# Kernel tuning notes

Measured on AMD Instinct MI355X. Metric: run time of the kernel, lower is better.

Reference implementation:

```python
import jax, jax.numpy as jnp
import numpy as np

N_NODES = 100_000
N_EDGES = 1_600_000
D_IN = 128
D_HID = 128
LN_EPS = 1e-5


def setup_inputs() -> dict:
    key = jax.random.key(0)
    k1, k2, k3 = jax.random.split(key, 3)
    x = jax.random.normal(k1, (N_NODES, D_IN), dtype=jnp.float32)
    edge_index = jax.random.randint(k2, (2, N_EDGES), 0, N_NODES, dtype=jnp.int32)
    # GCNConv linear weight (glorot-ish) and bias
    W = jax.random.normal(k3, (D_IN, D_HID), dtype=jnp.float32) * (1.0 / np.sqrt(D_IN))
    b = jnp.zeros((D_HID,), dtype=jnp.float32)
    # LayerNorm params
    gamma = jnp.ones((D_HID,), dtype=jnp.float32)
    beta = jnp.zeros((D_HID,), dtype=jnp.float32)
    return {"x": x, "edge_index": edge_index, "W": W, "b": b, "gamma": gamma, "beta": beta}


def reference(x, edge_index, W, b, gamma, beta):
    n = x.shape[0]
    # --- GCNConv: add self-loops, symmetric normalization ---
    loop = jnp.arange(n, dtype=edge_index.dtype)
    row = jnp.concatenate([edge_index[0], loop])  # source j
    col = jnp.concatenate([edge_index[1], loop])  # target i
    deg = jax.ops.segment_sum(jnp.ones(row.shape, x.dtype), col, num_segments=n)
    dinv = jnp.where(deg > 0, jax.lax.rsqrt(deg), jnp.zeros_like(deg))
    norm = dinv[row] * dinv[col]  # [E+N]
    # transform first (input->hidden), then gather-scale-scatter
    h = x @ W  # [N, D_HID]
    msg = h[row] * norm[:, None]  # gather + per-edge scale
    out = jax.ops.segment_sum(msg, col, num_segments=n) + b  # scatter-add
    # --- LayerNorm ---
    mu = jnp.mean(out, axis=-1, keepdims=True)
    var = jnp.mean(jnp.square(out - mu), axis=-1, keepdims=True)
    ln = (out - mu) * jax.lax.rsqrt(var + LN_EPS) * gamma + beta
    # Dropout is identity at inference; ReLU
    return jax.nn.relu(ln)
```

## Files before the change

### kernel.cpp

```cpp
#include <hip/hip_runtime.h>
#include <hip/hip_bf16.h>
#include <math.h>

#define LN_EPS 1e-5f
#define CAP 4096
#define CAPSH 12
#define NPBLK 576
#define ECHUNK 2816
#define MAXBUCK 800

typedef __attribute__((ext_vector_type(8))) short short8;
typedef __attribute__((ext_vector_type(4))) float floatx4;

__global__ __launch_bounds__(256) void k_init(const float* __restrict__ W, __hip_bfloat16* __restrict__ Wt,
                                              int* __restrict__ bucketCnt, unsigned* __restrict__ gdummy,
                                              float* __restrict__ dinv, int N) {
    int t = threadIdx.x;
    int i = blockIdx.x * 256 + t;
    int n = i >> 7, k = i & 127;
    Wt[i] = __float2bfloat16(W[k * 128 + n]);
    if (blockIdx.x == 0) {
        bucketCnt[t] = 0;
        bucketCnt[t + 256] = 0;
        bucketCnt[t + 512] = 0;
        bucketCnt[t + 768] = 0;
        if (t < 64) gdummy[t] = 0;
        if (t == 0) dinv[N] = 0.f;
    }
}

__global__ __launch_bounds__(256) void k_part_gemm(const int* __restrict__ ei, int* __restrict__ bucketCnt,
                                                   unsigned* __restrict__ pk, int E, int chunk,
                                                   const float* __restrict__ x, const __hip_bfloat16* __restrict__ Wt,
                                                   __hip_bfloat16* __restrict__ g, int N) {
    __shared__ union {
        struct { int ecol[ECHUNK]; int esrc[ECHUNK]; int h[MAXBUCK]; int base[MAXBUCK]; } part;
        unsigned short sB[128 * 128];
    } u;
    if ((int)blockIdx.x < NPBLK) {
        int t = threadIdx.x;
        for (int i = t; i < MAXBUCK; i += 256) u.part.h[i] = 0;
        int e0 = blockIdx.x * chunk;
        int e1 = min(e0 + chunk, E);
        int n = e1 - e0;
        __syncthreads();
        for (int i = t; i < n; i += 256) {
            int col = ei[E + e0 + i];
            u.part.ecol[i] = col;
            u.part.esrc[i] = ei[e0 + i];
            atomicAdd(&u.part.h[col >> 7], 1);
        }
        __syncthreads();
        for (int i = t; i < MAXBUCK; i += 256) {
            if (u.part.h[i] > 0) {
                u.part.base[i] = atomicAdd(&bucketCnt[i], u.part.h[i]);
                u.part.h[i] = 0;
            }
        }
        __syncthreads();
        for (int i = t; i < n; i += 256) {
            int col = u.part.ecol[i];
            int b = col >> 7;
            int r = u.part.base[b] + atomicAdd(&u.part.h[b], 1);
            if (r < CAP)
                pk[((unsigned)b << CAPSH) + r] = ((unsigned)(col & 127) << 20) | (unsigned)u.part.esrc[i];
        }
    } else {
        int tid = threadIdx.x;
        int row0 = ((int)blockIdx.x - NPBLK) * 128;
#pragma unroll
        for (int i = 0; i < 8; ++i) {
            int idx = tid + i * 256;
            int row = idx >> 4;
            int gr = idx & 15;
            int grs = gr ^ (row & 15);
            *(short8*)(&u.sB[row * 128 + grs * 8]) = *(const short8*)(Wt + (size_t)row * 128 + gr * 8);
        }
        __syncthreads();
        int lane = tid & 63;
        int wv = tid >> 6;
        int m = lane & 15;
        int q = lane >> 4;
        floatx4 acc[2][8];
#pragma unroll
        for (int mt = 0; mt < 2; ++mt)
#pragma unroll
            for (int nt = 0; nt < 8; ++nt) acc[mt][nt] = (floatx4){0.f, 0.f, 0.f, 0.f};
#pragma unroll
        for (int kc = 0; kc < 4; ++kc) {
            int gg = kc * 4 + q;
            short8 afrag[2], bfrag[8];
#pragma unroll
            for (int mt = 0; mt < 2; ++mt) {
                int arow = min(row0 + wv * 32 + mt * 16 + m, N - 1);
                const float* xp = x + (size_t)arow * 128 + gg * 8;
                float4 xa = *(const float4*)xp;
                float4 xb = *(const float4*)(xp + 4);
                union { short8 s; __hip_bfloat16 h[8]; } a;
                a.h[0] = __float2bfloat16(xa.x); a.h[1] = __float2bfloat16(xa.y);
                a.h[2] = __float2bfloat16(xa.z); a.h[3] = __float2bfloat16(xa.w);
                a.h[4] = __float2bfloat16(xb.x); a.h[5] = __float2bfloat16(xb.y);
                a.h[6] = __float2bfloat16(xb.z); a.h[7] = __float2bfloat16(xb.w);
                afrag[mt] = a.s;
            }
#pragma unroll
            for (int nt = 0; nt < 8; ++nt) {
                int n = nt * 16 + m;
                bfrag[nt] = *(const short8*)(&u.sB[n * 128 + (gg ^ (n & 15)) * 8]);
            }
#pragma unroll
            for (int mt = 0; mt < 2; ++mt)
#pragma unroll
                for (int nt = 0; nt < 8; ++nt)
                    acc[mt][nt] = __builtin_amdgcn_mfma_f32_16x16x32_bf16(afrag[mt], bfrag[nt], acc[mt][nt], 0, 0, 0);
        }
#pragma unroll
        for (int mt = 0; mt < 2; ++mt) {
#pragma unroll
            for (int i = 0; i < 4; ++i) {
                int row = row0 + wv * 32 + mt * 16 + q * 4 + i;
                if (row < N) {
                    __hip_bfloat16* gp = g + (size_t)row * 128;
#pragma unroll
                    for (int nt = 0; nt < 8; ++nt)
                        gp[nt * 16 + m] = __float2bfloat16(acc[mt][nt][i]);
                }
            }
        }
    }
}

__global__ __launch_bounds__(256) void k_csr(const unsigned* __restrict__ pk, const int* __restrict__ bucketCnt,
                                             int2* __restrict__ rowcnt, float* __restrict__ dinv,
                                             int* __restrict__ srcidx, int N) {
    __shared__ unsigned spk[CAP];
    __shared__ int lcnt[256];
    __shared__ int lofs[256];
    __shared__ int s[256];
    int b = blockIdx.x;
    int t = threadIdx.x;
    int ofs = b << CAPSH;
    int cntb = min(bucketCnt[b], CAP);
    lcnt[t] = 0;
    __syncthreads();
    for (int e = t; e < cntb; e += 256) {
        unsigned v = pk[ofs + e];
        spk[e] = v;
        atomicAdd(&lcnt[v >> 20], 1);
    }
    __syncthreads();
    int v = lcnt[t];
    int pv = (v + 7) & ~7;
    s[t] = pv;
    __syncthreads();
    int val = pv;
    for (int off = 1; off < 256; off <<= 1) {
        int add = (t >= off) ? s[t - off] : 0;
        __syncthreads();
        val += add;
        s[t] = val;
        __syncthreads();
    }
    lofs[t] = val - pv;
    int node = (b << 7) + t;
    if (t < 128 && node < N) {
        rowcnt[node] = make_int2(ofs + lofs[t], pv);
        dinv[node] = rsqrtf((float)(v + 1));
        for (int i = v; i < pv; ++i) {
            int slot = lofs[t] + i;
            if (slot < CAP) srcidx[ofs + slot] = N;
        }
    }
    lcnt[t] = 0;
    __syncthreads();
    for (int e = t; e < cntb; e += 256) {
        unsigned pvv = spk[e];
        int d = pvv >> 20;
        int r = atomicAdd(&lcnt[d], 1);
        int slot = lofs[d] + r;
        if (slot < CAP) srcidx[ofs + slot] = (int)(pvv & 0xFFFFFu);
    }
}

#define RLF(V, I) __int_as_float(__builtin_amdgcn_readlane(__float_as_int(V), (I)))

#define LOAD8(P, B) \
    unsigned P##0 = g1[((size_t)(unsigned)__builtin_amdgcn_readlane(myidx, (B) + 0)) * 64u + lane]; \
    unsigned P##1 = g1[((size_t)(unsigned)__builtin_amdgcn_readlane(myidx, (B) + 1)) * 64u + lane]; \
    unsigned P##2 = g1[((size_t)(unsigned)__builtin_amdgcn_readlane(myidx, (B) + 2)) * 64u + lane]; \
    unsigned P##3 = g1[((size_t)(unsigned)__builtin_amdgcn_readlane(myidx, (B) + 3)) * 64u + lane]; \
    unsigned P##4 = g1[((size_t)(unsigned)__builtin_amdgcn_readlane(myidx, (B) + 4)) * 64u + lane]; \
    unsigned P##5 = g1[((size_t)(unsigned)__builtin_amdgcn_readlane(myidx, (B) + 5)) * 64u + lane]; \
    unsigned P##6 = g1[((size_t)(unsigned)__builtin_amdgcn_readlane(myidx, (B) + 6)) * 64u + lane]; \
    unsigned P##7 = g1[((size_t)(unsigned)__builtin_amdgcn_readlane(myidx, (B) + 7)) * 64u + lane];

#define WACC8(P, B) { \
    float w0 = RLF(dlv, (B) + 0), w1 = RLF(dlv, (B) + 1), w2 = RLF(dlv, (B) + 2), w3 = RLF(dlv, (B) + 3); \
    float w4 = RLF(dlv, (B) + 4), w5 = RLF(dlv, (B) + 5), w6 = RLF(dlv, (B) + 6), w7 = RLF(dlv, (B) + 7); \
    ax += ((__uint_as_float(P##0 << 16) * w0 + __uint_as_float(P##1 << 16) * w1) + \
           (__uint_as_float(P##2 << 16) * w2 + __uint_as_float(P##3 << 16) * w3)) + \
          ((__uint_as_float(P##4 << 16) * w4 + __uint_as_float(P##5 << 16) * w5) + \
           (__uint_as_float(P##6 << 16) * w6 + __uint_as_float(P##7 << 16) * w7)); \
    ay += ((__uint_as_float(P##0 & 0xFFFF0000u) * w0 + __uint_as_float(P##1 & 0xFFFF0000u) * w1) + \
           (__uint_as_float(P##2 & 0xFFFF0000u) * w2 + __uint_as_float(P##3 & 0xFFFF0000u) * w3)) + \
          ((__uint_as_float(P##4 & 0xFFFF0000u) * w4 + __uint_as_float(P##5 & 0xFFFF0000u) * w5) + \
           (__uint_as_float(P##6 & 0xFFFF0000u) * w6 + __uint_as_float(P##7 & 0xFFFF0000u) * w7)); }

__global__ __launch_bounds__(256) void k_agg_ln(const __hip_bfloat16* __restrict__ g, const int* __restrict__ srcidx,
                                                const int2* __restrict__ rowcnt,
                                                const float* __restrict__ dinv, const float* __restrict__ bias,
                                                const float* __restrict__ gamma, const float* __restrict__ beta,
                                                float* __restrict__ out, int N) {
    int wid = (int)((blockIdx.x * 256u + threadIdx.x) >> 6);
    int lane = threadIdx.x & 63;
    if (wid >= N) return;
    const unsigned* g1 = (const unsigned*)g;
    float di = dinv[wid];
    unsigned sv = g1[(size_t)wid * 64 + lane];
    float ax = __uint_as_float(sv << 16) * di;
    float ay = __uint_as_float(sv & 0xFFFF0000u) * di;
    int2 rc = rowcnt[wid];
    int start = __builtin_amdgcn_readfirstlane(rc.x);
    int pcnt = __builtin_amdgcn_readfirstlane(rc.y);
    int end = start + pcnt;
    for (int eb = start; eb < end; eb += 64) {
        int myidx = srcidx[eb + lane];
        if (eb + lane >= end) myidx = N;
        float dlv = dinv[myidx];
        int nb = min(64, end - eb);
        if (nb >= 24) {
            LOAD8(pa, 0)
            LOAD8(pb, 8)
            LOAD8(pc, 16)
            WACC8(pa, 0)
            WACC8(pb, 8)
            WACC8(pc, 16)
            for (int j = 24; j + 8 <= nb; j += 8) {
                LOAD8(pd, j)
                WACC8(pd, j)
            }
        } else if (nb == 16) {
            LOAD8(pe, 0)
            LOAD8(pf, 8)
            WACC8(pe, 0)
            WACC8(pf, 8)
        } else {
            LOAD8(pg, 0)
            WACC8(pg, 0)
        }
    }
    float2 bi = ((const float2*)bias)[lane];
    float2 ga = ((const float2*)gamma)[lane];
    float2 be = ((const float2*)beta)[lane];
    float vx = ax * di + bi.x;
    float vy = ay * di + bi.y;
    float sum = vx + vy, sq = vx * vx + vy * vy;
#pragma unroll
    for (int off = 32; off > 0; off >>= 1) {
        sum += __shfl_xor(sum, off, 64);
        sq += __shfl_xor(sq, off, 64);
    }
    float mu = sum * (1.0f / 128.0f);
    float var = sq * (1.0f / 128.0f) - mu * mu;
    float rstd = rsqrtf(var + LN_EPS);
    float o0 = fmaxf((vx - mu) * rstd * ga.x + be.x, 0.f);
    float o1 = fmaxf((vy - mu) * rstd * ga.y + be.y, 0.f);
    ((float2*)out)[(size_t)wid * 64 + lane] = make_float2(o0, o1);
}

extern "C" void kernel_launch(void* const* d_in, const int* in_sizes, int n_in,
                              void* d_out, int out_size, void* d_ws, size_t ws_size,
                              hipStream_t stream) {
    const float* x = (const float*)d_in[0];
    const int* ei = (const int*)d_in[1];
    const float* W = (const float*)d_in[2];
    const float* bias = (const float*)d_in[3];
    const float* gamma = (const float*)d_in[4];
    const float* beta = (const float*)d_in[5];
    float* out = (float*)d_out;

    int N = in_sizes[0] / 128;
    int E = in_sizes[1] / 2;
    int NBUCK = (N + 127) / 128;

    char* p = (char*)d_ws;
    auto alloc = [&](size_t bytes) {
        char* r = p;
        p += (bytes + 255) & ~(size_t)255;
        return r;
    };
    int* bucketCnt = (int*)alloc(1024 * 4);
    int2* rowcnt = (int2*)alloc((size_t)N * 8);
    float* dinv = (float*)alloc((size_t)(N + 1) * 4);
    __hip_bfloat16* Wt = (__hip_bfloat16*)alloc(128 * 128 * 2);
    int* srcidx = (int*)alloc(((size_t)NBUCK * CAP + 64) * 4);
    __hip_bfloat16* gbuf = (__hip_bfloat16*)alloc((size_t)(N + 1) * 128 * 2);
    unsigned* pk = (unsigned*)d_out;

    int chunk = (E + NPBLK - 1) / NPBLK;
    int GB = (N + 127) / 128;

    k_init<<<64, 256, 0, stream>>>(W, Wt, bucketCnt, (unsigned*)(gbuf + (size_t)N * 128), dinv, N);
    k_part_gemm<<<NPBLK + GB, 256, 0, stream>>>(ei, bucketCnt, pk, E, chunk, x, Wt, gbuf, N);
    k_csr<<<NBUCK, 256, 0, stream>>>(pk, bucketCnt, rowcnt, dinv, srcidx, N);
    k_agg_ln<<<(N + 3) / 4, 256, 0, stream>>>(gbuf, srcidx, rowcnt, dinv, bias, gamma, beta, out, N);
}
```

Measured before the change: 211.6 us.

## Fuse per-bucket CSR build into aggregation kernel using shared-memory source indices

Result: no change. 214.6 us (+1.4%).

```diff
diff --git a/kernel.cpp b/kernel.cpp
--- a/kernel.cpp
+++ b/kernel.cpp
@@ -5,6 +5,7 @@
 #define LN_EPS 1e-5f
 #define CAP 4096
 #define CAPSH 12
+#define SIDXSZ (CAP + 896)
 #define NPBLK 576
 #define ECHUNK 2816
 #define MAXBUCK 800
@@ -130,55 +131,22 @@
     }
 }
 
-__global__ __launch_bounds__(256) void k_csr(const unsigned* __restrict__ pk, const int* __restrict__ bucketCnt,
-                                             int2* __restrict__ rowcnt, float* __restrict__ dinv,
-                                             int* __restrict__ srcidx, int N) {
-    __shared__ unsigned spk[CAP];
-    __shared__ int lcnt[256];
-    __shared__ int lofs[256];
-    __shared__ int s[256];
+__global__ __launch_bounds__(256) void k_deg(const unsigned* __restrict__ pk, const int* __restrict__ bucketCnt,
+                                             int* __restrict__ cnt, float* __restrict__ dinv, int N) {
+    __shared__ int lc[128];
     int b = blockIdx.x;
     int t = threadIdx.x;
+    if (t < 128) lc[t] = 0;
+    __syncthreads();
     int ofs = b << CAPSH;
     int cntb = min(bucketCnt[b], CAP);
-    lcnt[t] = 0;
-    __syncthreads();
-    for (int e = t; e < cntb; e += 256) {
-        unsigned v = pk[ofs + e];
-        spk[e] = v;
-        atomicAdd(&lcnt[v >> 20], 1);
-    }
-    __syncthreads();
-    int v = lcnt[t];
-    int pv = (v + 7) & ~7;
-    s[t] = pv;
-    __syncthreads();
-    int val = pv;
-    for (int off = 1; off < 256; off <<= 1) {
-        int add = (t >= off) ? s[t - off] : 0;
-        __syncthreads();
-        val += add;
-        s[t] = val;
-        __syncthreads();
-    }
-    lofs[t] = val - pv;
+    for (int e = t; e < cntb; e += 256)
+        atomicAdd(&lc[pk[ofs + e] >> 20], 1);
+    __syncthreads();
     int node = (b << 7) + t;
     if (t < 128 && node < N) {
-        rowcnt[node] = make_int2(ofs + lofs[t], pv);
-        dinv[node] = rsqrtf((float)(v + 1));
-        for (int i = v; i < pv; ++i) {
-            int slot = lofs[t] + i;
-            if (slot < CAP) srcidx[ofs + slot] = N;
-        }
-    }
-    lcnt[t] = 0;
-    __syncthreads();
-    for (int e = t; e < cntb; e += 256) {
-        unsigned pvv = spk[e];
-        int d = pvv >> 20;
-        int r = atomicAdd(&lcnt[d], 1);
-        int slot = lofs[d] + r;
-        if (slot < CAP) srcidx[ofs + slot] = (int)(pvv & 0xFFFFFu);
+        cnt[node] = lc[t];
+        dinv[node] = rsqrtf((float)(lc[t] + 1));
     }
 }
 
@@ -206,66 +174,108 @@
           ((__uint_as_float(P##4 & 0xFFFF0000u) * w4 + __uint_as_float(P##5 & 0xFFFF0000u) * w5) + \
            (__uint_as_float(P##6 & 0xFFFF0000u) * w6 + __uint_as_float(P##7 & 0xFFFF0000u) * w7)); }
 
-__global__ __launch_bounds__(256) void k_agg_ln(const __hip_bfloat16* __restrict__ g, const int* __restrict__ srcidx,
-                                                const int2* __restrict__ rowcnt,
+__global__ __launch_bounds__(256) void k_agg_ln(const __hip_bfloat16* __restrict__ g, const unsigned* __restrict__ pk,
+                                                const int* __restrict__ bucketCnt, const int* __restrict__ cnt,
                                                 const float* __restrict__ dinv, const float* __restrict__ bias,
                                                 const float* __restrict__ gamma, const float* __restrict__ beta,
                                                 float* __restrict__ out, int N) {
-    int wid = (int)((blockIdx.x * 256u + threadIdx.x) >> 6);
-    int lane = threadIdx.x & 63;
-    if (wid >= N) return;
+    __shared__ int sidx[SIDXSZ];
+    __shared__ int sscan[256];
+    __shared__ int lofs[128];
+    __shared__ int pvs[128];
+    __shared__ int lcnt[128];
+    int b = blockIdx.x;
+    int t = threadIdx.x;
+    int ofs = b << CAPSH;
+    int cntb = min(bucketCnt[b], CAP);
+    int nd = (b << 7) + t;
+    int v = (t < 128 && nd < N) ? cnt[nd] : 0;
+    int pv = (v + 7) & ~7;
+    sscan[t] = pv;
+    __syncthreads();
+    int val = pv;
+    for (int off = 1; off < 256; off <<= 1) {
+        int add = (t >= off) ? sscan[t - off] : 0;
+        __syncthreads();
+        val += add;
+        sscan[t] = val;
+        __syncthreads();
+    }
+    if (t < 128) {
+        int base = val - pv;
+        lofs[t] = base;
+        pvs[t] = pv;
+        lcnt[t] = 0;
+        for (int i = v; i < pv; ++i) {
+            int sl = base + i;
+            if (sl < SIDXSZ) sidx[sl] = N;
+        }
+    }
+    __syncthreads();
+    for (int e = t; e < cntb; e += 256) {
+        unsigned u = pk[ofs + e];
+        int d = u >> 20;
+        int r = atomicAdd(&lcnt[d], 1);
+        int sl = lofs[d] + r;
+        if (sl < SIDXSZ) sidx[sl] = (int)(u & 0xFFFFFu);
+    }
+    __syncthreads();
+    int lane = t & 63;
+    int wv = t >> 6;
     const unsigned* g1 = (const unsigned*)g;
-    float di = dinv[wid];
-    unsigned sv = g1[(size_t)wid * 64 + lane];
-    float ax = __uint_as_float(sv << 16) * di;
-    float ay = __uint_as_float(sv & 0xFFFF0000u) * di;
-    int2 rc = rowcnt[wid];
-    int start = __builtin_amdgcn_readfirstlane(rc.x);
-    int pcnt = __builtin_amdgcn_readfirstlane(rc.y);
-    int end = start + pcnt;
-    for (int eb = start; eb < end; eb += 64) {
-        int myidx = srcidx[eb + lane];
-        if (eb + lane >= end) myidx = N;
-        float dlv = dinv[myidx];
-        int nb = min(64, end - eb);
-        if (nb >= 24) {
-            LOAD8(pa, 0)
-            LOAD8(pb, 8)
-            LOAD8(pc, 16)
-            WACC8(pa, 0)
-            WACC8(pb, 8)
-            WACC8(pc, 16)
-            for (int j = 24; j + 8 <= nb; j += 8) {
-                LOAD8(pd, j)
-                WACC8(pd, j)
-            }
-        } else if (nb == 16) {
-            LOAD8(pe, 0)
-            LOAD8(pf, 8)
-            WACC8(pe, 0)
-            WACC8(pf, 8)
-        } else {
-            LOAD8(pg, 0)
-            WACC8(pg, 0)
-        }
-    }
     float2 bi = ((const float2*)bias)[lane];
     float2 ga = ((const float2*)gamma)[lane];
     float2 be = ((const float2*)beta)[lane];
-    float vx = ax * di + bi.x;
-    float vy = ay * di + bi.y;
-    float sum = vx + vy, sq = vx * vx + vy * vy;
-#pragma unroll
-    for (int off = 32; off > 0; off >>= 1) {
-        sum += __shfl_xor(sum, off, 64);
-        sq += __shfl_xor(sq, off, 64);
-    }
-    float mu = sum * (1.0f / 128.0f);
-    float var = sq * (1.0f / 128.0f) - mu * mu;
-    float rstd = rsqrtf(var + LN_EPS);
-    float o0 = fmaxf((vx - mu) * rstd * ga.x + be.x, 0.f);
-    float o1 = fmaxf((vy - mu) * rstd * ga.y + be.y, 0.f);
-    ((float2*)out)[(size_t)wid * 64 + lane] = make_float2(o0, o1);
+    for (int ii = 0; ii < 32; ++ii) {
+        int nl = wv * 32 + ii;
+        int node = (b << 7) + nl;
+        if (node >= N) break;
+        int startL = lofs[nl];
+        int endL = startL + pvs[nl];
+        float di = dinv[node];
+        unsigned sv = g1[(size_t)node * 64 + lane];
+        float ax = __uint_as_float(sv << 16) * di;
+        float ay = __uint_as_float(sv & 0xFFFF0000u) * di;
+        for (int eb = startL; eb < endL; eb += 64) {
+            int myidx = (eb + lane < endL) ? sidx[eb + lane] : N;
+            float dlv = dinv[myidx];
+            int nb = min(64, endL - eb);
+            if (nb >= 24) {
+                LOAD8(pa, 0)
+                LOAD8(pb, 8)
+                LOAD8(pc, 16)
+                WACC8(pa, 0)
+                WACC8(pb, 8)
+                WACC8(pc, 16)
+                for (int j = 24; j + 8 <= nb; j += 8) {
+                    LOAD8(pd, j)
+                    WACC8(pd, j)
+                }
+            } else if (nb == 16) {
+                LOAD8(pe, 0)
+                LOAD8(pf, 8)
+                WACC8(pe, 0)
+                WACC8(pf, 8)
+            } else {
+                LOAD8(pg, 0)
+                WACC8(pg, 0)
+            }
+        }
+        float vx = ax * di + bi.x;
+        float vy = ay * di + bi.y;
+        float sum = vx + vy, sq = vx * vx + vy * vy;
+#pragma unroll
+        for (int off = 32; off > 0; off >>= 1) {
+            sum += __shfl_xor(sum, off, 64);
+            sq += __shfl_xor(sq, off, 64);
+        }
+        float mu = sum * (1.0f / 128.0f);
+        float var = sq * (1.0f / 128.0f) - mu * mu;
+        float rstd = rsqrtf(var + LN_EPS);
+        float o0 = fmaxf((vx - mu) * rstd * ga.x + be.x, 0.f);
+        float o1 = fmaxf((vy - mu) * rstd * ga.y + be.y, 0.f);
+        ((float2*)out)[(size_t)node * 64 + lane] = make_float2(o0, o1);
+    }
 }
 
 extern "C" void kernel_launch(void* const* d_in, const int* in_sizes, int n_in,
@@ -290,18 +300,17 @@
         return r;
     };
     int* bucketCnt = (int*)alloc(1024 * 4);
-    int2* rowcnt = (int2*)alloc((size_t)N * 8);
+    int* cnt = (int*)alloc((size_t)N * 4);
     float* dinv = (float*)alloc((size_t)(N + 1) * 4);
     __hip_bfloat16* Wt = (__hip_bfloat16*)alloc(128 * 128 * 2);
-    int* srcidx = (int*)alloc(((size_t)NBUCK * CAP + 64) * 4);
+    unsigned* pk = (unsigned*)alloc((size_t)NBUCK * CAP * 4);
     __hip_bfloat16* gbuf = (__hip_bfloat16*)alloc((size_t)(N + 1) * 128 * 2);
-    unsigned* pk = (unsigned*)d_out;
 
     int chunk = (E + NPBLK - 1) / NPBLK;
     int GB = (N + 127) / 128;
 
     k_init<<<64, 256, 0, stream>>>(W, Wt, bucketCnt, (unsigned*)(gbuf + (size_t)N * 128), dinv, N);
     k_part_gemm<<<NPBLK + GB, 256, 0, stream>>>(ei, bucketCnt, pk, E, chunk, x, Wt, gbuf, N);
-    k_csr<<<NBUCK, 256, 0, stream>>>(pk, bucketCnt, rowcnt, dinv, srcidx, N);
-    k_agg_ln<<<(N + 3) / 4, 256, 0, stream>>>(gbuf, srcidx, rowcnt, dinv, bias, gamma, beta, out, N);
-}
+    k_deg<<<NBUCK, 256, 0, stream>>>(pk, bucketCnt, cnt, dinv, N);
+    k_agg_ln<<<NBUCK, 256, 0, stream>>>(gbuf, pk, bucketCnt, cnt, dinv, bias, gamma, beta, out, N);
+}
```
